# Optimization experiments

Measured on AMD Instinct MI355X. Metric: run time of the kernel, lower is better.

## Reference

```python
import jax, jax.numpy as jnp
import numpy as np

LRELU_SLOPE = 0.2
EPS = 1e-6

def _conv1x1(x, w):
    # x: [B,C,N,K], w: [O,C] -> [B,O,N,K]
    return jnp.einsum('bcnk,oc->bonk', x, w)

def _affine(x, g, b):
    # eval-mode BatchNorm with running mean=0, var=1 -> pure affine
    return x * g[None, :, None, None] + b[None, :, None, None]

def _lrelu(x):
    return jnp.where(x >= 0, x, LRELU_SLOPE * x)

def _head(x, w1, g, b, w2, b2):
    # Conv2d(2C,8,1,no bias) -> BN -> LeakyReLU -> (Dropout=id) -> Conv2d(8,1,1,bias)
    h = _lrelu(_affine(_conv1x1(x, w1), g, b))
    return _conv1x1(h, w2) + b2[None, :, None, None]  # [B,1,N,K]

def setup_inputs() -> dict:
    key = jax.random.key(0)
    ks = jax.random.split(key, 16)
    B, C2, N, K, O, H = 8, 128, 4096, 32, 64, 8
    inp = {
        'x': jax.random.normal(ks[0], (B, C2, N, K), jnp.float32),
        'w_trans': jax.random.normal(ks[1], (O, C2), jnp.float32) * 0.05,
        'g_trans': jax.random.uniform(ks[2], (O,), jnp.float32) + 0.5,
        'b_trans': jax.random.normal(ks[3], (O,), jnp.float32) * 0.1,
        'w_gate1': jax.random.normal(ks[4], (H, C2), jnp.float32) * 0.05,
        'g_gate': jax.random.uniform(ks[5], (H,), jnp.float32) + 0.5,
        'b_gate': jax.random.normal(ks[6], (H,), jnp.float32) * 0.1,
        'w_gate2': jax.random.normal(ks[7], (1, H), jnp.float32) * 0.3,
        'b_gate2': jax.random.normal(ks[8], (1,), jnp.float32) * 0.1,
        'w_attn1': jax.random.normal(ks[9], (H, C2), jnp.float32) * 0.05,
        'g_attn': jax.random.uniform(ks[10], (H,), jnp.float32) + 0.5,
        'b_attn': jax.random.normal(ks[11], (H,), jnp.float32) * 0.1,
        'w_attn2': jax.random.normal(ks[12], (1, H), jnp.float32) * 0.3,
        'b_attn2': jax.random.normal(ks[13], (1,), jnp.float32) * 0.1,
        'agg_alpha': jnp.zeros((), jnp.float32),
    }
    return inp

def reference(x, w_trans, g_trans, b_trans, w_gate1, g_gate, b_gate, w_gate2, b_gate2,
              w_attn1, g_attn, b_attn, w_attn2, b_attn2, agg_alpha):
    # mode='full', eval mode, tau=1.0, hard=False
    trans_feat = _lrelu(_affine(_conv1x1(x, w_trans), g_trans, b_trans))  # [B,O,N,K]
    gate_logits = _head(x, w_gate1, g_gate, b_gate, w_gate2, b_gate2)     # [B,1,N,K]
    # eval-mode gumbel_sigmoid_sample -> deterministic binary mask
    mask = (gate_logits >= 0).astype(x.dtype)                             # [B,1,N,K]
    attn_logits = _head(x, w_attn1, g_attn, b_attn, w_attn2, b_attn2)     # [B,1,N,K]
    attn_logits = attn_logits - jnp.max(attn_logits, axis=-1, keepdims=True)
    weights = jax.nn.softmax(attn_logits, axis=-1)
    # soft (hard=False) path: mask then renormalize
    weights = weights * mask
    weights = weights / (jnp.sum(weights, axis=-1, keepdims=True) + EPS)
    out_sum = jnp.sum(trans_feat * weights, axis=-1)   # [B,O,N]
    out_max = jnp.max(trans_feat, axis=-1)             # [B,O,N] (no masking when hard=False)
    alpha = jax.nn.sigmoid(agg_alpha)
    out = alpha * out_sum + (1.0 - alpha) * out_max
    return out, gate_logits
```

## Files before the change

kernel.cpp:

```cpp
#include <hip/hip_runtime.h>
#include <math.h>

#define NPB 131072
#define LRELU_SLOPE 0.2f
#define EPSV 1e-6f

typedef __attribute__((ext_vector_type(8))) short short8;
typedef __attribute__((ext_vector_type(4))) float f32x4;

static __device__ __forceinline__ unsigned short f2bf_rne(float f) {
    unsigned int u = __float_as_uint(f);
    u += 0x7fffu + ((u >> 16) & 1u);
    return (unsigned short)(u >> 16);
}

__global__ __launch_bounds__(256) void wt_kernel(
    const float* __restrict__ w_trans,
    const float* __restrict__ w_gate1,
    const float* __restrict__ w_attn1,
    unsigned short* __restrict__ Whi,
    unsigned short* __restrict__ Wlo)
{
    int i = blockIdx.x * 256 + threadIdx.x;
    if (i >= 80 * 128) return;
    int o = i >> 7;
    int c = i & 127;
    float v;
    if (o < 64)      v = w_trans[o * 128 + c];
    else if (o < 72) v = w_gate1[(o - 64) * 128 + c];
    else             v = w_attn1[(o - 72) * 128 + c];
    unsigned int u = __float_as_uint(v);
    Whi[i] = (unsigned short)(u >> 16);
    float hif = __uint_as_float(u & 0xffff0000u);
    Wlo[i] = f2bf_rne(v - hif);
}

__global__ __launch_bounds__(256, 3) void gsl_kernel(
    const float* __restrict__ x,
    const unsigned short* __restrict__ Whi,
    const unsigned short* __restrict__ Wlo,
    const float* __restrict__ g_trans, const float* __restrict__ b_trans,
    const float* __restrict__ g_gate,  const float* __restrict__ b_gate,
    const float* __restrict__ w_gate2, const float* __restrict__ b_gate2,
    const float* __restrict__ g_attn,  const float* __restrict__ b_attn,
    const float* __restrict__ w_attn2, const float* __restrict__ b_attn2,
    const float* __restrict__ agg_alpha,
    float* __restrict__ out0,
    float* __restrict__ outg)
{
    const int tid  = threadIdx.x;
    const int wid  = tid >> 6;
    const int lane = tid & 63;
    const int g    = lane >> 4;
    const int col  = lane & 15;

    const size_t p0 = (size_t)blockIdx.x * 128 + (size_t)wid * 32;
    const int b   = (int)(p0 >> 17);
    const int pin = (int)(p0 & (NPB - 1));
    const int n   = pin >> 5;

    const float* xq = x + (size_t)b * 128 * NPB + pin + col;

    f32x4 acc[5][2];
#pragma unroll
    for (int ot = 0; ot < 5; ++ot) {
        acc[ot][0] = (f32x4){0.f, 0.f, 0.f, 0.f};
        acc[ot][1] = (f32x4){0.f, 0.f, 0.f, 0.f};
    }

    float cur[16];
    {
        const int cb = 8 * g;
#pragma unroll
        for (int j = 0; j < 8; ++j) cur[j]     = xq[(size_t)(cb + j) * NPB];
#pragma unroll
        for (int j = 0; j < 8; ++j) cur[8 + j] = xq[(size_t)(cb + j) * NPB + 16];
    }

#pragma unroll 1
    for (int kk = 0; kk < 4; ++kk) {
        const int cbase = kk * 32 + 8 * g;

        float nxt[16];
        if (kk < 3) {
            const int cb2 = cbase + 32;
#pragma unroll
            for (int j = 0; j < 8; ++j) nxt[j]     = xq[(size_t)(cb2 + j) * NPB];
#pragma unroll
            for (int j = 0; j < 8; ++j) nxt[8 + j] = xq[(size_t)(cb2 + j) * NPB + 16];
        }

        short8 ahi[5], alo5[5];
#pragma unroll
        for (int ot = 0; ot < 5; ++ot) {
            const int wof = (ot * 16 + col) * 128 + cbase;
            ahi[ot]  = *(const short8*)(Whi + wof);
            alo5[ot] = *(const short8*)(Wlo + wof);
        }

        union U { unsigned int u[4]; short8 s; };
        U bh0, bl0, bh1, bl1;
#pragma unroll
        for (int jj = 0; jj < 4; ++jj) {
            float a0 = cur[2 * jj], a1 = cur[2 * jj + 1];
            unsigned int ua0 = __float_as_uint(a0), ua1 = __float_as_uint(a1);
            bh0.u[jj] = (ua1 & 0xffff0000u) | (ua0 >> 16);
            float r0 = a0 - __uint_as_float(ua0 & 0xffff0000u);
            float r1 = a1 - __uint_as_float(ua1 & 0xffff0000u);
            bl0.u[jj] = ((unsigned int)f2bf_rne(r1) << 16) | (unsigned int)f2bf_rne(r0);

            float c0v = cur[8 + 2 * jj], c1v = cur[8 + 2 * jj + 1];
            unsigned int uc0 = __float_as_uint(c0v), uc1 = __float_as_uint(c1v);
            bh1.u[jj] = (uc1 & 0xffff0000u) | (uc0 >> 16);
            float s0 = c0v - __uint_as_float(uc0 & 0xffff0000u);
            float s1v = c1v - __uint_as_float(uc1 & 0xffff0000u);
            bl1.u[jj] = ((unsigned int)f2bf_rne(s1v) << 16) | (unsigned int)f2bf_rne(s0);
        }

#pragma unroll
        for (int ot = 0; ot < 5; ++ot) {
            acc[ot][0] = __builtin_amdgcn_mfma_f32_16x16x32_bf16(ahi[ot],  bh0.s, acc[ot][0], 0, 0, 0);
            acc[ot][1] = __builtin_amdgcn_mfma_f32_16x16x32_bf16(ahi[ot],  bh1.s, acc[ot][1], 0, 0, 0);
            acc[ot][0] = __builtin_amdgcn_mfma_f32_16x16x32_bf16(alo5[ot], bh0.s, acc[ot][0], 0, 0, 0);
            acc[ot][1] = __builtin_amdgcn_mfma_f32_16x16x32_bf16(alo5[ot], bh1.s, acc[ot][1], 0, 0, 0);
            acc[ot][0] = __builtin_amdgcn_mfma_f32_16x16x32_bf16(ahi[ot],  bl0.s, acc[ot][0], 0, 0, 0);
            acc[ot][1] = __builtin_amdgcn_mfma_f32_16x16x32_bf16(ahi[ot],  bl1.s, acc[ot][1], 0, 0, 0);
        }

        if (kk < 3) {
#pragma unroll
            for (int j = 0; j < 16; ++j) cur[j] = nxt[j];
        }
    }

    const bool isGate = (g < 2);
    const int hbase = (g & 1) * 4;
    float hg[4], hb[4], hw[4];
#pragma unroll
    for (int r = 0; r < 4; ++r) {
        const int h = hbase + r;
        hg[r] = isGate ? g_gate[h]  : g_attn[h];
        hb[r] = isGate ? b_gate[h]  : b_attn[h];
        hw[r] = isGate ? w_gate2[h] : w_attn2[h];
    }
    float part0 = 0.f, part1 = 0.f;
#pragma unroll
    for (int r = 0; r < 4; ++r) {
        float v0 = fmaf(acc[4][0][r], hg[r], hb[r]);
        v0 = (v0 >= 0.f) ? v0 : LRELU_SLOPE * v0;
        part0 = fmaf(hw[r], v0, part0);
        float v1 = fmaf(acc[4][1][r], hg[r], hb[r]);
        v1 = (v1 >= 0.f) ? v1 : LRELU_SLOPE * v1;
        part1 = fmaf(hw[r], v1, part1);
    }
    float t0 = part0 + __shfl_xor(part0, 16);
    float t1 = part1 + __shfl_xor(part1, 16);
    float q0 = __shfl_xor(t0, 32);
    float q1 = __shfl_xor(t1, 32);
    const float bg2 = b_gate2[0], ba2 = b_attn2[0];
    float gl0 = (isGate ? t0 : q0) + bg2;
    float gl1 = (isGate ? t1 : q1) + bg2;
    float al0 = (isGate ? q0 : t0) + ba2;
    float al1 = (isGate ? q1 : t1) + ba2;

    if (lane < 16) {
        outg[p0 + col]      = gl0;
        outg[p0 + 16 + col] = gl1;
    }

    float m = fmaxf(al0, al1);
#pragma unroll
    for (int s = 1; s < 16; s <<= 1) m = fmaxf(m, __shfl_xor(m, s));
    float e0 = expf(al0 - m), e1 = expf(al1 - m);
    float w0m = (gl0 >= 0.f) ? e0 : 0.f;
    float w1m = (gl1 >= 0.f) ? e1 : 0.f;
    float s1 = e0 + e1;
    float sm = w0m + w1m;
#pragma unroll
    for (int s = 1; s < 16; s <<= 1) {
        s1 += __shfl_xor(s1, s);
        sm += __shfl_xor(sm, s);
    }
    const float inv = 1.f / (sm + EPSV * s1);
    const float wgt0 = w0m * inv;
    const float wgt1 = w1m * inv;

    const float aa = agg_alpha[0];
    const float alpha = 1.f / (1.f + expf(-aa));
    const float beta  = 1.f - alpha;

    float* outb = out0 + (size_t)b * 64 * 4096 + n;
#pragma unroll
    for (int ot = 0; ot < 4; ++ot) {
#pragma unroll
        for (int r = 0; r < 4; ++r) {
            const int o = ot * 16 + 4 * g + r;
            const float gt = g_trans[o], bt = b_trans[o];
            float v0 = fmaf(acc[ot][0][r], gt, bt);
            v0 = (v0 >= 0.f) ? v0 : LRELU_SLOPE * v0;
            float v1 = fmaf(acc[ot][1][r], gt, bt);
            v1 = (v1 >= 0.f) ? v1 : LRELU_SLOPE * v1;
            float sv = fmaf(v0, wgt0, v1 * wgt1);
            float mv = fmaxf(v0, v1);
#pragma unroll
            for (int s = 1; s < 16; s <<= 1) {
                sv += __shfl_xor(sv, s);
                mv = fmaxf(mv, __shfl_xor(mv, s));
            }
            if (col == 0)
                outb[(size_t)o * 4096] = fmaf(alpha, sv, beta * mv);
        }
    }
}

extern "C" void kernel_launch(void* const* d_in, const int* in_sizes, int n_in,
                              void* d_out, int out_size, void* d_ws, size_t ws_size,
                              hipStream_t stream) {
    const float* x        = (const float*)d_in[0];
    const float* w_trans  = (const float*)d_in[1];
    const float* g_trans  = (const float*)d_in[2];
    const float* b_trans  = (const float*)d_in[3];
    const float* w_gate1  = (const float*)d_in[4];
    const float* g_gate   = (const float*)d_in[5];
    const float* b_gate   = (const float*)d_in[6];
    const float* w_gate2  = (const float*)d_in[7];
    const float* b_gate2  = (const float*)d_in[8];
    const float* w_attn1  = (const float*)d_in[9];
    const float* g_attn   = (const float*)d_in[10];
    const float* b_attn   = (const float*)d_in[11];
    const float* w_attn2  = (const float*)d_in[12];
    const float* b_attn2  = (const float*)d_in[13];
    const float* agg_alpha= (const float*)d_in[14];

    float* out0 = (float*)d_out;
    float* outg = (float*)d_out + (size_t)8*64*4096;
    unsigned short* Whi = (unsigned short*)d_ws;
    unsigned short* Wlo = Whi + 80 * 128;

    wt_kernel<<<(80*128 + 255)/256, 256, 0, stream>>>(w_trans, w_gate1, w_attn1, Whi, Wlo);

    const int npix = 8 * NPB;
    gsl_kernel<<<npix / 128, 256, 0, stream>>>(
        x, Whi, Wlo, g_trans, b_trans, g_gate, b_gate, w_gate2, b_gate2,
        g_attn, b_attn, w_attn2, b_attn2, agg_alpha, out0, outg);
}
```

Before: 837.0 us.

## Drop manual x prefetch, fully unroll K loop, raise occupancy, use packed bf16 converts

Removes the explicit double-buffered register prefetch of x, fully unrolls the 4-step channel loop, and raises the launch-bounds occupancy hint from 3 to 4 blocks per CU. The bf16 hi/lo split now uses v_perm for the high halves and a packed RNE float-to-bf16 conversion for the low residuals, replacing manual bit manipulation. The aim is to lower register pressure so more waves can hide the memory-bound x loads, and to cut ALU work in the split. The risk is that the compiler schedules loads less well than the manual prefetch, or spills under the tighter register limit.

Result: no change. 821.1 us (-1.9%).

```diff
diff --git a/kernel.cpp b/kernel.cpp
--- a/kernel.cpp
+++ b/kernel.cpp
@@ -1,4 +1,5 @@
 #include <hip/hip_runtime.h>
+#include <hip/hip_bf16.h>
 #include <math.h>
 
 #define NPB 131072
@@ -12,6 +13,13 @@
     unsigned int u = __float_as_uint(f);
     u += 0x7fffu + ((u >> 16) & 1u);
     return (unsigned short)(u >> 16);
+}
+
+static __device__ __forceinline__ unsigned int cvt_pk_bf16(float f0, float f1) {
+    __hip_bfloat162 h = __float22bfloat162_rn(make_float2(f0, f1));
+    unsigned int r;
+    __builtin_memcpy(&r, &h, 4);
+    return r;
 }
 
 __global__ __launch_bounds__(256) void wt_kernel(
@@ -35,7 +43,7 @@
     Wlo[i] = f2bf_rne(v - hif);
 }
 
-__global__ __launch_bounds__(256, 3) void gsl_kernel(
+__global__ __launch_bounds__(256, 4) void gsl_kernel(
     const float* __restrict__ x,
     const unsigned short* __restrict__ Whi,
     const unsigned short* __restrict__ Wlo,
@@ -68,68 +76,44 @@
         acc[ot][1] = (f32x4){0.f, 0.f, 0.f, 0.f};
     }
 
-    float cur[16];
-    {
-        const int cb = 8 * g;
-#pragma unroll
-        for (int j = 0; j < 8; ++j) cur[j]     = xq[(size_t)(cb + j) * NPB];
-#pragma unroll
-        for (int j = 0; j < 8; ++j) cur[8 + j] = xq[(size_t)(cb + j) * NPB + 16];
-    }
-
-#pragma unroll 1
+#pragma unroll
     for (int kk = 0; kk < 4; ++kk) {
         const int cbase = kk * 32 + 8 * g;
 
-        float nxt[16];
-        if (kk < 3) {
-            const int cb2 = cbase + 32;
-#pragma unroll
-            for (int j = 0; j < 8; ++j) nxt[j]     = xq[(size_t)(cb2 + j) * NPB];
-#pragma unroll
-            for (int j = 0; j < 8; ++j) nxt[8 + j] = xq[(size_t)(cb2 + j) * NPB + 16];
+        float xv[16];
+#pragma unroll
+        for (int j = 0; j < 8; ++j) xv[j]     = xq[(size_t)(cbase + j) * NPB];
+#pragma unroll
+        for (int j = 0; j < 8; ++j) xv[8 + j] = xq[(size_t)(cbase + j) * NPB + 16];
+
+        union U { unsigned int u[4]; short8 s; };
+        U bh0, bl0, bh1, bl1;
+#pragma unroll
+        for (int jj = 0; jj < 4; ++jj) {
+            float a0 = xv[2 * jj], a1 = xv[2 * jj + 1];
+            unsigned int ua0 = __float_as_uint(a0), ua1 = __float_as_uint(a1);
+            bh0.u[jj] = __builtin_amdgcn_perm(ua1, ua0, 0x07060302u);
+            bl0.u[jj] = cvt_pk_bf16(a0 - __uint_as_float(ua0 & 0xffff0000u),
+                                    a1 - __uint_as_float(ua1 & 0xffff0000u));
+
+            float c0v = xv[8 + 2 * jj], c1v = xv[8 + 2 * jj + 1];
+            unsigned int uc0 = __float_as_uint(c0v), uc1 = __float_as_uint(c1v);
+            bh1.u[jj] = __builtin_amdgcn_perm(uc1, uc0, 0x07060302u);
+            bl1.u[jj] = cvt_pk_bf16(c0v - __uint_as_float(uc0 & 0xffff0000u),
+                                    c1v - __uint_as_float(uc1 & 0xffff0000u));
         }
 
-        short8 ahi[5], alo5[5];
 #pragma unroll
         for (int ot = 0; ot < 5; ++ot) {
             const int wof = (ot * 16 + col) * 128 + cbase;
-            ahi[ot]  = *(const short8*)(Whi + wof);
-            alo5[ot] = *(const short8*)(Wlo + wof);
-        }
-
-        union U { unsigned int u[4]; short8 s; };
-        U bh0, bl0, bh1, bl1;
-#pragma unroll
-        for (int jj = 0; jj < 4; ++jj) {
-            float a0 = cur[2 * jj], a1 = cur[2 * jj + 1];
-            unsigned int ua0 = __float_as_uint(a0), ua1 = __float_as_uint(a1);
-            bh0.u[jj] = (ua1 & 0xffff0000u) | (ua0 >> 16);
-            float r0 = a0 - __uint_as_float(ua0 & 0xffff0000u);
-            float r1 = a1 - __uint_as_float(ua1 & 0xffff0000u);
-            bl0.u[jj] = ((unsigned int)f2bf_rne(r1) << 16) | (unsigned int)f2bf_rne(r0);
-
-            float c0v = cur[8 + 2 * jj], c1v = cur[8 + 2 * jj + 1];
-            unsigned int uc0 = __float_as_uint(c0v), uc1 = __float_as_uint(c1v);
-            bh1.u[jj] = (uc1 & 0xffff0000u) | (uc0 >> 16);
-            float s0 = c0v - __uint_as_float(uc0 & 0xffff0000u);
-            float s1v = c1v - __uint_as_float(uc1 & 0xffff0000u);
-            bl1.u[jj] = ((unsigned int)f2bf_rne(s1v) << 16) | (unsigned int)f2bf_rne(s0);
-        }
-
-#pragma unroll
-        for (int ot = 0; ot < 5; ++ot) {
-            acc[ot][0] = __builtin_amdgcn_mfma_f32_16x16x32_bf16(ahi[ot],  bh0.s, acc[ot][0], 0, 0, 0);
-            acc[ot][1] = __builtin_amdgcn_mfma_f32_16x16x32_bf16(ahi[ot],  bh1.s, acc[ot][1], 0, 0, 0);
-            acc[ot][0] = __builtin_amdgcn_mfma_f32_16x16x32_bf16(alo5[ot], bh0.s, acc[ot][0], 0, 0, 0);
-            acc[ot][1] = __builtin_amdgcn_mfma_f32_16x16x32_bf16(alo5[ot], bh1.s, acc[ot][1], 0, 0, 0);
-            acc[ot][0] = __builtin_amdgcn_mfma_f32_16x16x32_bf16(ahi[ot],  bl0.s, acc[ot][0], 0, 0, 0);
-            acc[ot][1] = __builtin_amdgcn_mfma_f32_16x16x32_bf16(ahi[ot],  bl1.s, acc[ot][1], 0, 0, 0);
-        }
-
-        if (kk < 3) {
-#pragma unroll
-            for (int j = 0; j < 16; ++j) cur[j] = nxt[j];
+            short8 ahi = *(const short8*)(Whi + wof);
+            short8 alo = *(const short8*)(Wlo + wof);
+            acc[ot][0] = __builtin_amdgcn_mfma_f32_16x16x32_bf16(ahi, bh0.s, acc[ot][0], 0, 0, 0);
+            acc[ot][1] = __builtin_amdgcn_mfma_f32_16x16x32_bf16(ahi, bh1.s, acc[ot][1], 0, 0, 0);
+            acc[ot][0] = __builtin_amdgcn_mfma_f32_16x16x32_bf16(alo, bh0.s, acc[ot][0], 0, 0, 0);
+            acc[ot][1] = __builtin_amdgcn_mfma_f32_16x16x32_bf16(alo, bh1.s, acc[ot][1], 0, 0, 0);
+            acc[ot][0] = __builtin_amdgcn_mfma_f32_16x16x32_bf16(ahi, bl0.s, acc[ot][0], 0, 0, 0);
+            acc[ot][1] = __builtin_amdgcn_mfma_f32_16x16x32_bf16(ahi, bl1.s, acc[ot][1], 0, 0, 0);
         }
     }
 
```
